# Optimization experiments

Measured on AMD Instinct MI355X. Metric: run time of the kernel, lower is better.

## Reference

```python
import jax, jax.numpy as jnp
import numpy as np


def log_g(x):
    # log of g(x) = where(x>=0, x+0.5, sigmoid(x)), computed stably in log space
    return jnp.where(x >= 0.0, jnp.log(jax.nn.relu(x) + 0.5), -jax.nn.softplus(-x))


def setup_inputs() -> dict:
    key = jax.random.key(0)
    k1, k2, k3 = jax.random.split(key, 3)
    B, T, D = 4, 4096, 512
    D_inner = 4 * D  # expansion_factor = 4.0
    x = jax.random.normal(k1, (B, T, D), dtype=jnp.float32)
    # torch Linear weights: W_hg [2*D_inner, D], W_out [D, D_inner]
    W_hg = jax.random.normal(k2, (2 * D_inner, D), dtype=jnp.float32) * 0.02
    b_hg = jnp.zeros((2 * D_inner,), dtype=jnp.float32)
    W_out = jax.random.normal(k3, (D, D_inner), dtype=jnp.float32) * 0.02
    b_out = jnp.zeros((D,), dtype=jnp.float32)
    return {"x": x, "W_hg": W_hg, "b_hg": b_hg, "W_out": W_out, "b_out": b_out}


def reference(x, W_hg, b_hg, W_out, b_out):
    # x: [B, T, D]
    hg = jnp.einsum('btd,ed->bte', x, W_hg) + b_hg          # [B, T, 2*D_inner]
    hidden, gate = jnp.split(hg, 2, axis=-1)                # each [B, T, D_inner]

    log_coeffs = -jax.nn.softplus(gate)                     # log a_t = log sigmoid(-gate)... = log(1-z)
    log_z = -jax.nn.softplus(-gate)                         # log z_t = log sigmoid(gate)
    log_values = log_z + log_g(hidden)                      # log b_t

    # pad one step at front of time axis (prev_hidden=None path: padded log value 0)
    pad = ((0, 0), (1, 0), (0, 0))
    log_coeffs_p = jnp.pad(log_coeffs, pad)                 # [B, T+1, D_inner]
    log_values_p = jnp.pad(log_values, pad)

    # Heinsen log-space associative scan
    a_star = jnp.cumsum(log_coeffs_p, axis=1)
    log_h = a_star + jax.lax.cumlogsumexp(log_values_p - a_star, axis=1)
    h = jnp.exp(log_h)[:, 1:, :]                            # [B, T, D_inner]

    out = jnp.einsum('bte,de->btd', h, W_out) + b_out       # [B, T, D]
    return out
```

## Files before the change

### kernel.cpp

```cpp
#include <hip/hip_runtime.h>
#include <hip/hip_bf16.h>

#define B_   4
#define T_   4096
#define D_   512
#define E_   2048
#define M_   (B_*T_)
#define N1_  (2*E_)
#define K1_  D_
#define N2_  D_
#define K2_  E_
#define CT_  128
#define NC_  (T_/CT_)

typedef __attribute__((ext_vector_type(8))) short short8_t;
typedef __attribute__((ext_vector_type(4))) float f32x4;

__device__ inline unsigned short f2bf(float f){
  unsigned u = __float_as_uint(f);
  u += 0x7fffu + ((u >> 16) & 1u);
  return (unsigned short)(u >> 16);
}
__device__ inline float bf2f(unsigned h){ return __uint_as_float(h << 16); }

__global__ __launch_bounds__(256) void conv_f32_bf16_x4(const float* __restrict__ in,
                                                        short* __restrict__ out, int n4){
  int i = blockIdx.x * 256 + threadIdx.x;
  if (i >= n4) return;
  float4 v = ((const float4*)in)[i];
  short4 o;
  o.x = (short)f2bf(v.x); o.y = (short)f2bf(v.y);
  o.z = (short)f2bf(v.z); o.w = (short)f2bf(v.w);
  ((short4*)out)[i] = o;
}

__global__ __launch_bounds__(128) void conv_whg(const float* __restrict__ W,
                                                short* __restrict__ Wp){
  int r = blockIdx.x;
  int e = ((r >> 6) << 5) + (r & 31);
  int orig = e + ((r >> 5) & 1) * E_;
  float4 v = ((const float4*)(W + (size_t)orig * K1_))[threadIdx.x];
  short4 o;
  o.x = (short)f2bf(v.x); o.y = (short)f2bf(v.y);
  o.z = (short)f2bf(v.z); o.w = (short)f2bf(v.w);
  ((short4*)(Wp + (size_t)r * K1_))[threadIdx.x] = o;
}

template<int EPI>
__global__ __launch_bounds__(256)
void gemm_bt(const short* __restrict__ A, const short* __restrict__ Bmat, int K,
             const float* __restrict__ bias,
             unsigned* __restrict__ ab_out,
             float* __restrict__ c_out, int ldc)
{
  __shared__ short As[128 * 64];
  __shared__ short Bs[128 * 64];
  const int tid  = threadIdx.x;
  const int lane = tid & 63;
  const int w    = tid >> 6;
  const int wr   = (w >> 1) * 64;
  const int wc   = (w & 1) * 64;

  const int nwg = gridDim.x * gridDim.y;
  const int lin = blockIdx.y * gridDim.x + blockIdx.x;
  const int nl  = (lin & 7) * (nwg >> 3) + (lin >> 3);
  const int brow = (nl / gridDim.x) * 128;
  const int bcol = (nl % gridDim.x) * 128;

  f32x4 acc[4][4];
  #pragma unroll
  for (int m = 0; m < 4; ++m)
    #pragma unroll
    for (int n = 0; n < 4; ++n) acc[m][n] = (f32x4){0.f, 0.f, 0.f, 0.f};

  const int srow = lane >> 3;
  const int scol = ((lane & 7) ^ srow) * 8;
  const int l15  = lane & 15;
  const int kh   = (lane >> 4) * 8;
  const int sw   = (l15 & 7) << 3;

  for (int kt = 0; kt < K; kt += 64) {
    #pragma unroll
    for (int i = 0; i < 4; ++i) {
      const int rr = (w * 4 + i) * 8 + srow;
      const short* ga = A    + (size_t)(brow + rr) * K + kt + scol;
      const short* gb = Bmat + (size_t)(bcol + rr) * K + kt + scol;
      __builtin_amdgcn_global_load_lds((const __attribute__((address_space(1))) void*)ga,
                                       (__attribute__((address_space(3))) void*)(As + (w * 4 + i) * 512),
                                       16, 0, 0);
      __builtin_amdgcn_global_load_lds((const __attribute__((address_space(1))) void*)gb,
                                       (__attribute__((address_space(3))) void*)(Bs + (w * 4 + i) * 512),
                                       16, 0, 0);
    }
    __syncthreads();
    #pragma unroll
    for (int kk = 0; kk < 64; kk += 32) {
      short8_t af[4], bf[4];
      #pragma unroll
      for (int m = 0; m < 4; ++m)
        af[m] = *(const short8_t*)(As + (wr + m * 16 + l15) * 64 + ((kk + kh) ^ sw));
      #pragma unroll
      for (int n = 0; n < 4; ++n)
        bf[n] = *(const short8_t*)(Bs + (wc + n * 16 + l15) * 64 + ((kk + kh) ^ sw));
      #pragma unroll
      for (int m = 0; m < 4; ++m)
        #pragma unroll
        for (int n = 0; n < 4; ++n)
          acc[m][n] = __builtin_amdgcn_mfma_f32_16x16x32_bf16(af[m], bf[n], acc[m][n], 0, 0, 0);
    }
    __syncthreads();
  }

  const int r4 = (lane >> 4) * 4;
  if constexpr (EPI == 0) {
    const int ebase = (bcol + wc) >> 1;
    #pragma unroll
    for (int m = 0; m < 4; ++m) {
      const int row = brow + wr + m * 16 + r4;
      #pragma unroll
      for (int n = 0; n < 2; ++n) {
        const int e = ebase + n * 16 + l15;
        const float bh = bias[e];
        const float bg = bias[E_ + e];
        #pragma unroll
        for (int j = 0; j < 4; ++j) {
          float hh = acc[m][n][j]     + bh;
          float gg = acc[m][n + 2][j] + bg;
          float mabs = fabsf(gg);
          float em   = __expf(-mabs);
          float inv  = 1.f / (1.f + em);
          float z = (gg >= 0.f) ? inv : em * inv;
          float a = (gg >= 0.f) ? em * inv : inv;
          float gf = (hh >= 0.f) ? (hh + 0.5f) : (1.f / (1.f + __expf(-hh)));
          float bb = z * gf;
          unsigned pk = ((unsigned)f2bf(bb) << 16) | (unsigned)f2bf(a);
          ab_out[(size_t)(row + j) * E_ + e] = pk;
        }
      }
    }
  } else {
    #pragma unroll
    for (int m = 0; m < 4; ++m) {
      #pragma unroll
      for (int n = 0; n < 4; ++n) {
        const int row = brow + wr + m * 16 + r4;
        const int col = bcol + wc + n * 16 + l15;
        #pragma unroll
        for (int j = 0; j < 4; ++j)
          c_out[(size_t)(row + j) * ldc + col] = acc[m][n][j] + bias[col];
      }
    }
  }
}

__global__ __launch_bounds__(256) void scan_chunk(const unsigned* __restrict__ ab,
                                                  float* __restrict__ Ac,
                                                  float* __restrict__ Bc){
  const int c = blockIdx.x;
  const int e = (blockIdx.y * 256 + threadIdx.x) * 4;
  const int b = blockIdx.z;
  size_t base = (((size_t)b * T_ + (size_t)c * CT_) * E_ + e) >> 2;
  const uint4* abv = (const uint4*)ab;
  float A0=1.f,A1=1.f,A2=1.f,A3=1.f, H0=0.f,H1=0.f,H2=0.f,H3=0.f;
  #pragma unroll 4
  for (int t = 0; t < CT_; ++t) {
    uint4 wv = abv[base + (size_t)t * (E_ / 4)];
    float a0=bf2f(wv.x&0xffffu), b0=bf2f(wv.x>>16);
    float a1=bf2f(wv.y&0xffffu), b1=bf2f(wv.y>>16);
    float a2=bf2f(wv.z&0xffffu), b2=bf2f(wv.z>>16);
    float a3=bf2f(wv.w&0xffffu), b3=bf2f(wv.w>>16);
    H0=fmaf(a0,H0,b0); H1=fmaf(a1,H1,b1); H2=fmaf(a2,H2,b2); H3=fmaf(a3,H3,b3);
    A0*=a0; A1*=a1; A2*=a2; A3*=a3;
  }
  size_t ci = (((size_t)b * NC_ + c) * E_ + e) >> 2;
  ((float4*)Ac)[ci] = (float4){A0,A1,A2,A3};
  ((float4*)Bc)[ci] = (float4){H0,H1,H2,H3};
}

__global__ __launch_bounds__(256) void scan_carry(const float* __restrict__ Ac,
                                                  const float* __restrict__ Bc,
                                                  float* __restrict__ Hc){
  int idx = blockIdx.x * 256 + threadIdx.x;
  int b = idx >> 11;
  int e = idx & (E_ - 1);
  float H = 1.f;
  for (int c = 0; c < NC_; ++c) {
    size_t ci = ((size_t)b * NC_ + c) * E_ + e;
    float A = Ac[ci], Bv = Bc[ci];
    Hc[ci] = H;
    H = fmaf(A, H, Bv);
  }
}

__global__ __launch_bounds__(256) void scan_final(const unsigned* __restrict__ ab,
                                                  const float* __restrict__ Hc,
                                                  short* __restrict__ h){
  const int c = blockIdx.x;
  const int e = (blockIdx.y * 256 + threadIdx.x) * 4;
  const int b = blockIdx.z;
  size_t base = (((size_t)b * T_ + (size_t)c * CT_) * E_ + e) >> 2;
  const uint4* abv = (const uint4*)ab;
  float4 Hv = ((const float4*)Hc)[(((size_t)b * NC_ + c) * E_ + e) >> 2];
  float H0=Hv.x, H1=Hv.y, H2=Hv.z, H3=Hv.w;
  short4* hv = (short4*)h;
  #pragma unroll 4
  for (int t = 0; t < CT_; ++t) {
    uint4 wv = abv[base + (size_t)t * (E_ / 4)];
    H0 = fmaf(bf2f(wv.x&0xffffu), H0, bf2f(wv.x>>16));
    H1 = fmaf(bf2f(wv.y&0xffffu), H1, bf2f(wv.y>>16));
    H2 = fmaf(bf2f(wv.z&0xffffu), H2, bf2f(wv.z>>16));
    H3 = fmaf(bf2f(wv.w&0xffffu), H3, bf2f(wv.w>>16));
    short4 o;
    o.x=(short)f2bf(H0); o.y=(short)f2bf(H1); o.z=(short)f2bf(H2); o.w=(short)f2bf(H3);
    hv[base + (size_t)t * (E_ / 4)] = o;
  }
}

extern "C" void kernel_launch(void* const* d_in, const int* in_sizes, int n_in,
                              void* d_out, int out_size, void* d_ws, size_t ws_size,
                              hipStream_t stream)
{
  const float* x     = (const float*)d_in[0];
  const float* W_hg  = (const float*)d_in[1];
  const float* b_hg  = (const float*)d_in[2];
  const float* W_out = (const float*)d_in[3];
  const float* b_out = (const float*)d_in[4];
  float* out = (float*)d_out;

  char* p = (char*)d_ws;
  auto carve = [&](size_t bytes) -> char* {
    char* q = p; p += (bytes + 255) & ~(size_t)255; return q;
  };
  short*    xb   = (short*)   carve((size_t)M_ * K1_ * 2);
  short*    Wp   = (short*)   carve((size_t)N1_ * K1_ * 2);
  short*    Wo   = (short*)   carve((size_t)N2_ * K2_ * 2);
  unsigned* ab   = (unsigned*)carve((size_t)M_ * E_ * 4);
  short*    hbuf = (short*)   carve((size_t)M_ * E_ * 2);
  float*    Ac   = (float*)   carve((size_t)B_ * NC_ * E_ * 4);
  float*    Bc   = (float*)   carve((size_t)B_ * NC_ * E_ * 4);
  float*    Hc   = (float*)   carve((size_t)B_ * NC_ * E_ * 4);

  conv_f32_bf16_x4<<<(M_ * K1_ / 4 + 255) / 256, 256, 0, stream>>>(x, xb, M_ * K1_ / 4);
  conv_whg<<<N1_, 128, 0, stream>>>(W_hg, Wp);
  conv_f32_bf16_x4<<<(N2_ * K2_ / 4 + 255) / 256, 256, 0, stream>>>(W_out, Wo, N2_ * K2_ / 4);

  gemm_bt<0><<<dim3(N1_ / 128, M_ / 128), 256, 0, stream>>>(xb, Wp, K1_, b_hg, ab, nullptr, 0);

  scan_chunk<<<dim3(NC_, E_ / 1024, B_), 256, 0, stream>>>(ab, Ac, Bc);
  scan_carry<<<(B_ * E_) / 256, 256, 0, stream>>>(Ac, Bc, Hc);
  scan_final<<<dim3(NC_, E_ / 1024, B_), 256, 0, stream>>>(ab, Hc, hbuf);

  gemm_bt<1><<<dim3(N2_ / 128, M_ / 128), 256, 0, stream>>>(hbuf, Wo, K2_, b_out, nullptr, out, N2_);
}
```

Baseline: 304.3 us.

## Replace first GEMM with 256x256-tile 8-wave double-buffered pipelined kernel

The input projection GEMM moves to a new kernel. It uses 256x256 output tiles, 512 threads (8 waves) and double-buffered LDS filled with global_load_lds. Loads are interleaved with MFMA quads under explicit vmcnt waits, barriers and s_setprio, so global→LDS traffic overlaps compute and per-tile data reuse goes up. The fused gating epilogue stays the same, and the old templated GEMM is reduced to the output-projection case. In exchange, LDS use rises to 128KB per block and register pressure grows, which limits each CU to a single resident block.

```diff
diff --git a/kernel.cpp b/kernel.cpp
--- a/kernel.cpp
+++ b/kernel.cpp
@@ -23,6 +23,16 @@
 }
 __device__ inline float bf2f(unsigned h){ return __uint_as_float(h << 16); }
 
+#define STG(gp, lp) __builtin_amdgcn_global_load_lds( \
+    (const __attribute__((address_space(1))) void*)(gp), \
+    (__attribute__((address_space(3))) void*)(lp), 16, 0, 0)
+#define BAR()   __builtin_amdgcn_s_barrier()
+#define LGKM0() asm volatile("s_waitcnt lgkmcnt(0)" ::: "memory")
+#define VM4()   asm volatile("s_waitcnt vmcnt(4)" ::: "memory")
+#define VM0()   asm volatile("s_waitcnt vmcnt(0)" ::: "memory")
+#define PRIO1() __builtin_amdgcn_s_setprio(1)
+#define PRIO0() __builtin_amdgcn_s_setprio(0)
+
 __global__ __launch_bounds__(256) void conv_f32_bf16_x4(const float* __restrict__ in,
                                                         short* __restrict__ out, int n4){
   int i = blockIdx.x * 256 + threadIdx.x;
@@ -46,12 +56,145 @@
   ((short4*)(Wp + (size_t)r * K1_))[threadIdx.x] = o;
 }
 
-template<int EPI>
+template<int KK>
+__global__ __launch_bounds__(512, 2)
+void gemm8p_ab(const short* __restrict__ A, const short* __restrict__ Bmat,
+               const float* __restrict__ bias, unsigned* __restrict__ ab_out)
+{
+  __shared__ short As[2][256 * 64];
+  __shared__ short Bs[2][256 * 64];
+  constexpr int NT = KK / 64, NI = NT / 2;
+
+  const int tid = threadIdx.x;
+  const int lane = tid & 63;
+  const int w   = tid >> 6;
+  const int wm  = w >> 2;
+  const int wn  = w & 3;
+  const int l15 = lane & 15;
+  const int kh  = (lane >> 4) * 8;
+  const int swz = (l15 & 7) << 3;
+
+  const int nwg = gridDim.x * gridDim.y;
+  const int lin = blockIdx.y * gridDim.x + blockIdx.x;
+  const int nl  = (lin & 7) * (nwg >> 3) + (lin >> 3);
+  const int brow = (nl / gridDim.x) * 256;
+  const int bcol = (nl % gridDim.x) * 256;
+
+  const int srow8 = lane >> 3;
+  const int scol  = ((lane & 7) ^ srow8) * 8;
+  const short *gA0[2], *gA1[2], *gB0[2], *gB1[2];
+  #pragma unroll
+  for (int h = 0; h < 2; ++h) {
+    gA0[h] = A    + (size_t)(brow + h * 128 + w * 16 + srow8) * KK + scol;
+    gA1[h] = gA0[h] + 8 * KK;
+    gB0[h] = Bmat + (size_t)(bcol + h * 128 + w * 16 + srow8) * KK + scol;
+    gB1[h] = gB0[h] + 8 * KK;
+  }
+  auto stgA = [&](int db, int h, int kt) {
+    STG(gA0[h] + kt, &As[db][(h * 128 + w * 16) * 64]);
+    STG(gA1[h] + kt, &As[db][(h * 128 + w * 16 + 8) * 64]);
+  };
+  auto stgB = [&](int db, int h, int kt) {
+    STG(gB0[h] + kt, &Bs[db][(h * 128 + w * 16) * 64]);
+    STG(gB1[h] + kt, &Bs[db][(h * 128 + w * 16 + 8) * 64]);
+  };
+
+  f32x4 acc[8][4];
+  #pragma unroll
+  for (int m = 0; m < 8; ++m)
+    #pragma unroll
+    for (int n = 0; n < 4; ++n) acc[m][n] = (f32x4){0.f, 0.f, 0.f, 0.f};
+
+  short8_t af[4][2], bf[4][2];
+  auto LDA4 = [&](int db, int qr) {
+    #pragma unroll
+    for (int i = 0; i < 4; ++i) {
+      const int rb = (wm * 128 + qr * 64 + i * 16 + l15) * 64;
+      af[i][0] = *(const short8_t*)&As[db][rb + (kh ^ swz)];
+      af[i][1] = *(const short8_t*)&As[db][rb + ((32 + kh) ^ swz)];
+    }
+  };
+  auto LDB2 = [&](int db, int hf) {
+    #pragma unroll
+    for (int n = 0; n < 2; ++n) {
+      const int rb = (wn * 64 + (hf * 2 + n) * 16 + l15) * 64;
+      bf[hf * 2 + n][0] = *(const short8_t*)&Bs[db][rb + (kh ^ swz)];
+      bf[hf * 2 + n][1] = *(const short8_t*)&Bs[db][rb + ((32 + kh) ^ swz)];
+    }
+  };
+  auto QUAD = [&](int ar, int bn) {
+    #pragma unroll
+    for (int kk = 0; kk < 2; ++kk)
+      #pragma unroll
+      for (int i = 0; i < 4; ++i)
+        #pragma unroll
+        for (int n = 0; n < 2; ++n)
+          acc[ar + i][bn + n] = __builtin_amdgcn_mfma_f32_16x16x32_bf16(
+              af[i][kk], bf[bn + n][kk], acc[ar + i][bn + n], 0, 0, 0);
+  };
+
+  stgA(0, 0, 0); stgA(0, 1, 0); stgB(0, 0, 0); stgB(0, 1, 0);
+  stgB(1, 0, 64); stgB(1, 1, 64);
+  VM4(); BAR();
+
+  for (int j = 0; j < NI; ++j) {
+    const bool last = (j == NI - 1);
+    const int ktB1 = (2 * j + 1) * 64;
+    const int ktN0 = (2 * j + 2) * 64;
+    const int ktN1 = (2 * j + 3) * 64;
+    LDA4(0, 0); LDB2(0, 0); stgA(1, 0, ktB1);
+    BAR(); LGKM0(); PRIO1(); QUAD(0, 0); PRIO0(); BAR();
+    LDB2(0, 1); stgA(1, 1, ktB1);
+    BAR(); LGKM0(); PRIO1(); QUAD(0, 2); PRIO0(); BAR();
+    LDA4(0, 1); if (!last) stgB(0, 0, ktN0);
+    BAR(); LGKM0(); PRIO1(); QUAD(4, 0); PRIO0(); BAR();
+    if (!last) stgB(0, 1, ktN0);
+    BAR(); LGKM0(); PRIO1(); QUAD(4, 2); PRIO0();
+    if (last) { VM0(); } else { VM4(); }
+    BAR();
+    LDA4(1, 0); LDB2(1, 0); if (!last) stgA(0, 0, ktN0);
+    BAR(); LGKM0(); PRIO1(); QUAD(0, 0); PRIO0(); BAR();
+    LDB2(1, 1); if (!last) stgA(0, 1, ktN0);
+    BAR(); LGKM0(); PRIO1(); QUAD(0, 2); PRIO0(); BAR();
+    LDA4(1, 1); if (!last) stgB(1, 0, ktN1);
+    BAR(); LGKM0(); PRIO1(); QUAD(4, 0); PRIO0(); BAR();
+    if (!last) stgB(1, 1, ktN1);
+    BAR(); LGKM0(); PRIO1(); QUAD(4, 2); PRIO0();
+    if (!last) { VM4(); }
+    BAR();
+  }
+
+  const int r4 = (lane >> 4) * 4;
+  const int ebase = (bcol + wn * 64) >> 1;
+  #pragma unroll
+  for (int ar = 0; ar < 8; ++ar) {
+    const int row = brow + wm * 128 + ar * 16 + r4;
+    #pragma unroll
+    for (int bn = 0; bn < 2; ++bn) {
+      const int e = ebase + bn * 16 + l15;
+      const float bh = bias[e];
+      const float bg = bias[E_ + e];
+      #pragma unroll
+      for (int jj = 0; jj < 4; ++jj) {
+        float hh = acc[ar][bn][jj]     + bh;
+        float gg = acc[ar][bn + 2][jj] + bg;
+        float mabs = fabsf(gg);
+        float em   = __expf(-mabs);
+        float inv  = 1.f / (1.f + em);
+        float z = (gg >= 0.f) ? inv : em * inv;
+        float a = (gg >= 0.f) ? em * inv : inv;
+        float gf = (hh >= 0.f) ? (hh + 0.5f) : (1.f / (1.f + __expf(-hh)));
+        float bb = z * gf;
+        unsigned pk = ((unsigned)f2bf(bb) << 16) | (unsigned)f2bf(a);
+        ab_out[(size_t)(row + jj) * E_ + e] = pk;
+      }
+    }
+  }
+}
+
 __global__ __launch_bounds__(256)
 void gemm_bt(const short* __restrict__ A, const short* __restrict__ Bmat, int K,
-             const float* __restrict__ bias,
-             unsigned* __restrict__ ab_out,
-             float* __restrict__ c_out, int ldc)
+             const float* __restrict__ bias, float* __restrict__ c_out, int ldc)
 {
   __shared__ short As[128 * 64];
   __shared__ short Bs[128 * 64];
@@ -85,70 +228,38 @@
       const int rr = (w * 4 + i) * 8 + srow;
       const short* ga = A    + (size_t)(brow + rr) * K + kt + scol;
       const short* gb = Bmat + (size_t)(bcol + rr) * K + kt + scol;
-      __builtin_amdgcn_global_load_lds((const __attribute__((address_space(1))) void*)ga,
-                                       (__attribute__((address_space(3))) void*)(As + (w * 4 + i) * 512),
-                                       16, 0, 0);
-      __builtin_amdgcn_global_load_lds((const __attribute__((address_space(1))) void*)gb,
-                                       (__attribute__((address_space(3))) void*)(Bs + (w * 4 + i) * 512),
-                                       16, 0, 0);
+      STG(ga, As + (w * 4 + i) * 512);
+      STG(gb, Bs + (w * 4 + i) * 512);
     }
     __syncthreads();
     #pragma unroll
     for (int kk = 0; kk < 64; kk += 32) {
-      short8_t af[4], bf[4];
+      short8_t afr[4], bfr[4];
       #pragma unroll
       for (int m = 0; m < 4; ++m)
-        af[m] = *(const short8_t*)(As + (wr + m * 16 + l15) * 64 + ((kk + kh) ^ sw));
+        afr[m] = *(const short8_t*)(As + (wr + m * 16 + l15) * 64 + ((kk + kh) ^ sw));
       #pragma unroll
       for (int n = 0; n < 4; ++n)
-        bf[n] = *(const short8_t*)(Bs + (wc + n * 16 + l15) * 64 + ((kk + kh) ^ sw));
+        bfr[n] = *(const short8_t*)(Bs + (wc + n * 16 + l15) * 64 + ((kk + kh) ^ sw));
       #pragma unroll
       for (int m = 0; m < 4; ++m)
         #pragma unroll
         for (int n = 0; n < 4; ++n)
-          acc[m][n] = __builtin_amdgcn_mfma_f32_16x16x32_bf16(af[m], bf[n], acc[m][n], 0, 0, 0);
+          acc[m][n] = __builtin_amdgcn_mfma_f32_16x16x32_bf16(afr[m], bfr[n], acc[m][n], 0, 0, 0);
     }
     __syncthreads();
   }
 
   const int r4 = (lane >> 4) * 4;
-  if constexpr (EPI == 0) {
-    const int ebase = (bcol + wc) >> 1;
-    #pragma unroll
-    for (int m = 0; m < 4; ++m) {
+  #pragma unroll
+  for (int m = 0; m < 4; ++m) {
+    #pragma unroll
+    for (int n = 0; n < 4; ++n) {
       const int row = brow + wr + m * 16 + r4;
-      #pragma unroll
-      for (int n = 0; n < 2; ++n) {
-        const int e = ebase + n * 16 + l15;
-        const float bh = bias[e];
-        const float bg = bias[E_ + e];
-        #pragma unroll
-        for (int j = 0; j < 4; ++j) {
-          float hh = acc[m][n][j]     + bh;
-          float gg = acc[m][n + 2][j] + bg;
-          float mabs = fabsf(gg);
-          float em   = __expf(-mabs);
-          float inv  = 1.f / (1.f + em);
-          float z = (gg >= 0.f) ? inv : em * inv;
-          float a = (gg >= 0.f) ? em * inv : inv;
-          float gf = (hh >= 0.f) ? (hh + 0.5f) : (1.f / (1.f + __expf(-hh)));
-          float bb = z * gf;
-          unsigned pk = ((unsigned)f2bf(bb) << 16) | (unsigned)f2bf(a);
-          ab_out[(size_t)(row + j) * E_ + e] = pk;
-        }
-      }
-    }
-  } else {
-    #pragma unroll
-    for (int m = 0; m < 4; ++m) {
-      #pragma unroll
-      for (int n = 0; n < 4; ++n) {
-        const int row = brow + wr + m * 16 + r4;
-        const int col = bcol + wc + n * 16 + l15;
-        #pragma unroll
-        for (int j = 0; j < 4; ++j)
-          c_out[(size_t)(row + j) * ldc + col] = acc[m][n][j] + bias[col];
-      }
+      const int col = bcol + wc + n * 16 + l15;
+      #pragma unroll
+      for (int j = 0; j < 4; ++j)
+        c_out[(size_t)(row + j) * ldc + col] = acc[m][n][j] + bias[col];
     }
   }
 }
@@ -244,11 +355,11 @@
   conv_whg<<<N1_, 128, 0, stream>>>(W_hg, Wp);
   conv_f32_bf16_x4<<<(N2_ * K2_ / 4 + 255) / 256, 256, 0, stream>>>(W_out, Wo, N2_ * K2_ / 4);
 
-  gemm_bt<0><<<dim3(N1_ / 128, M_ / 128), 256, 0, stream>>>(xb, Wp, K1_, b_hg, ab, nullptr, 0);
+  gemm8p_ab<K1_><<<dim3(N1_ / 256, M_ / 256), 512, 0, stream>>>(xb, Wp, b_hg, ab);
 
   scan_chunk<<<dim3(NC_, E_ / 1024, B_), 256, 0, stream>>>(ab, Ac, Bc);
   scan_carry<<<(B_ * E_) / 256, 256, 0, stream>>>(Ac, Bc, Hc);
   scan_final<<<dim3(NC_, E_ / 1024, B_), 256, 0, stream>>>(ab, Hc, hbuf);
 
-  gemm_bt<1><<<dim3(N2_ / 128, M_ / 128), 256, 0, stream>>>(hbuf, Wo, K2_, b_out, nullptr, out, N2_);
-}
+  gemm_bt<<<dim3(N2_ / 128, M_ / 128), 256, 0, stream>>>(hbuf, Wo, K2_, b_out, out, N2_);
+}
```

New measurement: 301.1 us. About the same (-1.0%).

## Double-buffer LDS in GEMMs with compile-time K and cheaper gate epilogue

Applied to the files above, without the earlier changes.

Both GEMMs move to a double-buffered LDS scheme. The next K tile's global-to-LDS loads are issued before the current tile's MFMAs, which cuts one barrier per iteration and overlaps memory with compute. K becomes a template parameter, so the k-loop fully unrolls with precomputed base pointers, and launch bounds ask for 2 blocks per CU. The gate epilogue uses hardware reciprocal and packed bf16 conversion instructions in place of division and manual rounding, which may change rounding slightly. Doubled LDS (64KB per block) may limit occupancy.

```diff
diff --git a/kernel.cpp b/kernel.cpp
--- a/kernel.cpp
+++ b/kernel.cpp
@@ -1,5 +1,6 @@
 #include <hip/hip_runtime.h>
 #include <hip/hip_bf16.h>
+#include <type_traits>
 
 #define B_   4
 #define T_   4096
@@ -22,6 +23,17 @@
   return (unsigned short)(u >> 16);
 }
 __device__ inline float bf2f(unsigned h){ return __uint_as_float(h << 16); }
+__device__ inline float fast_rcp(float x){
+  float r; asm("v_rcp_f32 %0, %1" : "=v"(r) : "v"(x)); return r;
+}
+__device__ inline unsigned pk_bf16(float lo, float hi){
+  unsigned r; asm("v_cvt_pk_bf16_f32 %0, %1, %2" : "=v"(r) : "v"(lo), "v"(hi)); return r;
+}
+
+template<int I, int N, typename F>
+__device__ __forceinline__ void sfor(F&& f){
+  if constexpr (I < N) { f(std::integral_constant<int, I>{}); sfor<I + 1, N>(f); }
+}
 
 __global__ __launch_bounds__(256) void conv_f32_bf16_x4(const float* __restrict__ in,
                                                         short* __restrict__ out, int n4){
@@ -46,15 +58,17 @@
   ((short4*)(Wp + (size_t)r * K1_))[threadIdx.x] = o;
 }
 
-template<int EPI>
-__global__ __launch_bounds__(256)
-void gemm_bt(const short* __restrict__ A, const short* __restrict__ Bmat, int K,
+template<int EPI, int KK>
+__global__ __launch_bounds__(256, 2)
+void gemm_db(const short* __restrict__ A, const short* __restrict__ Bmat,
              const float* __restrict__ bias,
              unsigned* __restrict__ ab_out,
              float* __restrict__ c_out, int ldc)
 {
-  __shared__ short As[128 * 64];
-  __shared__ short Bs[128 * 64];
+  __shared__ short As[2][128 * 64];
+  __shared__ short Bs[2][128 * 64];
+  constexpr int NT = KK / 64;
+
   const int tid  = threadIdx.x;
   const int lane = tid & 63;
   const int w    = tid >> 6;
@@ -79,37 +93,57 @@
   const int kh   = (lane >> 4) * 8;
   const int sw   = (l15 & 7) << 3;
 
-  for (int kt = 0; kt < K; kt += 64) {
+  const short* ga[4]; const short* gb[4];
+  #pragma unroll
+  for (int i = 0; i < 4; ++i) {
+    const int rr = (w * 4 + i) * 8 + srow;
+    ga[i] = A    + (size_t)(brow + rr) * KK + scol;
+    gb[i] = Bmat + (size_t)(bcol + rr) * KK + scol;
+  }
+
+  auto stage = [&](auto CUR, auto TT) {
+    constexpr int cb = decltype(CUR)::value;
+    constexpr int kt = decltype(TT)::value * 64;
     #pragma unroll
     for (int i = 0; i < 4; ++i) {
-      const int rr = (w * 4 + i) * 8 + srow;
-      const short* ga = A    + (size_t)(brow + rr) * K + kt + scol;
-      const short* gb = Bmat + (size_t)(bcol + rr) * K + kt + scol;
-      __builtin_amdgcn_global_load_lds((const __attribute__((address_space(1))) void*)ga,
-                                       (__attribute__((address_space(3))) void*)(As + (w * 4 + i) * 512),
-                                       16, 0, 0);
-      __builtin_amdgcn_global_load_lds((const __attribute__((address_space(1))) void*)gb,
-                                       (__attribute__((address_space(3))) void*)(Bs + (w * 4 + i) * 512),
-                                       16, 0, 0);
-    }
-    __syncthreads();
+      __builtin_amdgcn_global_load_lds(
+          (const __attribute__((address_space(1))) void*)(ga[i] + kt),
+          (__attribute__((address_space(3))) void*)&As[cb][(w * 4 + i) * 512], 16, 0, 0);
+      __builtin_amdgcn_global_load_lds(
+          (const __attribute__((address_space(1))) void*)(gb[i] + kt),
+          (__attribute__((address_space(3))) void*)&Bs[cb][(w * 4 + i) * 512], 16, 0, 0);
+    }
+  };
+  auto comp = [&](auto CUR) {
+    constexpr int cb = decltype(CUR)::value;
     #pragma unroll
     for (int kk = 0; kk < 64; kk += 32) {
-      short8_t af[4], bf[4];
+      short8_t afr[4], bfr[4];
       #pragma unroll
       for (int m = 0; m < 4; ++m)
-        af[m] = *(const short8_t*)(As + (wr + m * 16 + l15) * 64 + ((kk + kh) ^ sw));
+        afr[m] = *(const short8_t*)&As[cb][(wr + m * 16 + l15) * 64 + ((kk + kh) ^ sw)];
       #pragma unroll
       for (int n = 0; n < 4; ++n)
-        bf[n] = *(const short8_t*)(Bs + (wc + n * 16 + l15) * 64 + ((kk + kh) ^ sw));
+        bfr[n] = *(const short8_t*)&Bs[cb][(wc + n * 16 + l15) * 64 + ((kk + kh) ^ sw)];
       #pragma unroll
       for (int m = 0; m < 4; ++m)
         #pragma unroll
         for (int n = 0; n < 4; ++n)
-          acc[m][n] = __builtin_amdgcn_mfma_f32_16x16x32_bf16(af[m], bf[n], acc[m][n], 0, 0, 0);
-    }
-    __syncthreads();
-  }
+          acc[m][n] = __builtin_amdgcn_mfma_f32_16x16x32_bf16(afr[m], bfr[n], acc[m][n], 0, 0, 0);
+    }
+  };
+
+  stage(std::integral_constant<int, 0>{}, std::integral_constant<int, 0>{});
+  __syncthreads();
+
+  sfor<0, NT>([&](auto TT) {
+    constexpr int t   = decltype(TT)::value;
+    constexpr int cur = t & 1;
+    if constexpr (t + 1 < NT)
+      stage(std::integral_constant<int, cur ^ 1>{}, std::integral_constant<int, t + 1>{});
+    comp(std::integral_constant<int, cur>{});
+    if constexpr (t + 1 < NT) __syncthreads();
+  });
 
   const int r4 = (lane >> 4) * 4;
   if constexpr (EPI == 0) {
@@ -126,15 +160,12 @@
         for (int j = 0; j < 4; ++j) {
           float hh = acc[m][n][j]     + bh;
           float gg = acc[m][n + 2][j] + bg;
-          float mabs = fabsf(gg);
-          float em   = __expf(-mabs);
-          float inv  = 1.f / (1.f + em);
-          float z = (gg >= 0.f) ? inv : em * inv;
-          float a = (gg >= 0.f) ? em * inv : inv;
-          float gf = (hh >= 0.f) ? (hh + 0.5f) : (1.f / (1.f + __expf(-hh)));
+          float r  = fast_rcp(1.f + __expf(-fabsf(gg)));
+          float z  = (gg >= 0.f) ? r : 1.f - r;
+          float a  = 1.f - z;
+          float gf = (hh >= 0.f) ? (hh + 0.5f) : fast_rcp(1.f + __expf(-hh));
           float bb = z * gf;
-          unsigned pk = ((unsigned)f2bf(bb) << 16) | (unsigned)f2bf(a);
-          ab_out[(size_t)(row + j) * E_ + e] = pk;
+          ab_out[(size_t)(row + j) * E_ + e] = pk_bf16(a, bb);
         }
       }
     }
@@ -244,11 +275,11 @@
   conv_whg<<<N1_, 128, 0, stream>>>(W_hg, Wp);
   conv_f32_bf16_x4<<<(N2_ * K2_ / 4 + 255) / 256, 256, 0, stream>>>(W_out, Wo, N2_ * K2_ / 4);
 
-  gemm_bt<0><<<dim3(N1_ / 128, M_ / 128), 256, 0, stream>>>(xb, Wp, K1_, b_hg, ab, nullptr, 0);
+  gemm_db<0, K1_><<<dim3(N1_ / 128, M_ / 128), 256, 0, stream>>>(xb, Wp, b_hg, ab, nullptr, 0);
 
   scan_chunk<<<dim3(NC_, E_ / 1024, B_), 256, 0, stream>>>(ab, Ac, Bc);
   scan_carry<<<(B_ * E_) / 256, 256, 0, stream>>>(Ac, Bc, Hc);
   scan_final<<<dim3(NC_, E_ / 1024, B_), 256, 0, stream>>>(ab, Hc, hbuf);
 
-  gemm_bt<1><<<dim3(N2_ / 128, M_ / 128), 256, 0, stream>>>(hbuf, Wo, K2_, b_out, nullptr, out, N2_);
-}
+  gemm_db<1, K2_><<<dim3(N2_ / 128, M_ / 128), 256, 0, stream>>>(hbuf, Wo, b_out, nullptr, out, N2_);
+}
```

After: 300.1 us. No clear change (-1.4%).
